# Optimization experiments

Hardware: AMD Instinct MI355X
Metric: run time of the kernel (lower is better)

## Reference

```python
import jax, jax.numpy as jnp
import numpy as np

B, IN_C, H, W = 32, 256, 32, 32
C_OUT, NUM_MODES, NEG_MODES, EMB = 256, 1, 3, 512
SIGMA, BETA, NEG_SCOPE, EPS = 0.5, 0.3, 2.0, 1e-12


def _l2norm(v, axis):
    return v / jnp.maximum(jnp.linalg.norm(v, axis=axis, keepdims=True), EPS)


def setup_inputs() -> dict:
    key = jax.random.key(0)
    ks = jax.random.split(key, 6)
    x = jax.random.normal(ks[0], (B, IN_C, H, W), jnp.float32)
    W_emb = jax.random.normal(ks[1], (EMB, IN_C), jnp.float32) * 0.02  # 1x1 conv kernel
    # rep_fc / neg_rep_fc: nn.Linear(1, C*modes*E), normal_init std=0.01
    rep_w = jax.random.normal(ks[2], (C_OUT * NUM_MODES * EMB, 1), jnp.float32) * 0.01
    rep_b = jax.random.normal(ks[3], (C_OUT * NUM_MODES * EMB,), jnp.float32) * 0.01
    neg_rep_w = jax.random.normal(ks[4], (C_OUT * NEG_MODES * EMB, 1), jnp.float32) * 0.01
    neg_rep_b = jax.random.normal(ks[5], (C_OUT * NEG_MODES * EMB,), jnp.float32) * 0.01
    return {"x": x, "W_emb": W_emb, "rep_w": rep_w, "rep_b": rep_b,
            "neg_rep_w": neg_rep_w, "neg_rep_b": neg_rep_b}


def reference(x, W_emb, rep_w, rep_b, neg_rep_w, neg_rep_b):
    # emb_module: 1x1 conv, then L2-normalize over channel dim (dim=1)
    emb = jnp.einsum('bchw,ec->behw', x, W_emb)
    emb = _l2norm(emb, axis=1)                                    # [B,E,H,W], unit-norm over E
    # training branch: reps = normalize(rep_fc(1.0)) = normalize(w*1 + b)
    reps = _l2norm((rep_w[:, 0] + rep_b).reshape(C_OUT, NUM_MODES, EMB), axis=2)
    reps_neg = _l2norm((neg_rep_w[:, 0] + neg_rep_b).reshape(C_OUT, NEG_MODES, EMB), axis=2)

    def dist(r):
        # ||e - r||^2 = ||e||^2 + ||r||^2 - 2 e.r = 2 - 2 e.r (both unit-norm)
        dot = jnp.einsum('behw,cme->bcmhw', emb, r)               # [B,C,M,H,W]
        return jnp.sqrt(jnp.maximum(2.0 - 2.0 * dot, 0.0))

    distances = dist(reps)                                        # [B,C,1,H,W]
    distances_neg = dist(reps_neg)                                # [B,C,3,H,W]
    inv2s2 = 1.0 / (2.0 * SIGMA ** 2)

    probs_neg = jnp.exp(-distances_neg ** 2 * inv2s2)
    cls_score_neg = probs_neg.max(axis=2)                         # [B,C,H,W]
    probs_ori = jnp.exp(-distances ** 2 * inv2s2).max(axis=2)     # [B,C,H,W]

    neg_min = distances_neg.min(axis=2, keepdims=True)            # [B,C,1,H,W]
    probs = jnp.exp(-(distances + BETA * jax.nn.relu(NEG_SCOPE - neg_min)) ** 2 * inv2s2)
    # cls_norm=True branch
    probs_sumj = probs.sum(axis=2)                                # [B,C,H,W]
    cls_score = probs_sumj / probs_sumj.sum(axis=1, keepdims=True)
    return (cls_score, cls_score_neg, distances, distances_neg, probs_ori)
```

## Files before the change

### kernel.cpp

```cpp
#include <hip/hip_runtime.h>
#include <stdint.h>

using s16x8 = __attribute__((ext_vector_type(8))) short;
using f32x4 = __attribute__((ext_vector_type(4))) float;

#define HW 1024
#define INC 256
#define EMB 512
#define NPX 32768

#define OFF_CS 0
#define OFF_CN 8388608
#define OFF_D  16777216
#define OFF_DN 25165824
#define OFF_PO 50331648

__device__ __forceinline__ uint32_t f2bf(float f) {
  uint32_t u = __float_as_uint(f);
  return (u + 0x7FFFu + ((u >> 16) & 1u)) >> 16;
}
__device__ __forceinline__ int lswz(int row, int byte) {
  return byte ^ (((row >> 2) & 7) << 4);
}

__global__ __launch_bounds__(64) void k_prep(
    const float* __restrict__ rep_w, const float* __restrict__ rep_b,
    const float* __restrict__ neg_w, const float* __restrict__ neg_b,
    uint16_t* __restrict__ R) {
  int rb = blockIdx.x, lane = threadIdx.x;
  int c = rb >> 2, md = rb & 3;
  const float* w  = (md == 0) ? rep_w : neg_w;
  const float* bb = (md == 0) ? rep_b : neg_b;
  int base = (md == 0) ? c * EMB : (c * 3 + md - 1) * EMB;
  float v[8]; float ss = 0.f;
#pragma unroll
  for (int j = 0; j < 8; ++j) {
    float t = w[base + lane * 8 + j] + bb[base + lane * 8 + j];
    v[j] = t; ss += t * t;
  }
#pragma unroll
  for (int o = 1; o < 64; o <<= 1) ss += __shfl_xor(ss, o, 64);
  float inv = 1.f / fmaxf(sqrtf(ss), 1e-12f);
  uint16_t* dst = R + rb * EMB + lane * 8;
#pragma unroll
  for (int j = 0; j < 8; ++j) dst[j] = (uint16_t)f2bf(v[j] * inv);
}

__global__ __launch_bounds__(256) void k_gemm1(
    const float* __restrict__ x, const float* __restrict__ wemb,
    uint16_t* __restrict__ emb, float* __restrict__ nparts) {
  int bid = blockIdx.x;
  int w = (bid & 7) * 128 + (bid >> 3);
  int e_tile = w & 3, px_tile = w >> 2;
  int e0 = e_tile * 128, px0 = px_tile * 128;
  int bimg = px0 >> 10, hw0 = px0 & 1023;
  int tid = threadIdx.x, lane = tid & 63, wid = tid >> 6;
  int wm = wid >> 1, wn = wid & 1, lr = lane & 15, lk = lane >> 4;
  __shared__ __align__(16) char smA[16384];
  __shared__ __align__(16) char smB[16384];
  f32x4 acc[4][4] = {};
  const float4* x4 = (const float4*)x;
  const float4* w4 = (const float4*)wemb;
  for (int kt = 0; kt < INC; kt += 64) {
    if (kt) __syncthreads();
#pragma unroll
    for (int i = 0; i < 4; ++i) {
      int p = tid + i * 256;
      int c2 = p >> 5, px4 = p & 31;
      int gi = ((bimg * INC + kt + c2 * 2) * HW + hw0) >> 2;
      float4 fa = x4[gi + px4];
      float4 fb = x4[gi + 256 + px4];
      float fa_[4] = {fa.x, fa.y, fa.z, fa.w};
      float fb_[4] = {fb.x, fb.y, fb.z, fb.w};
#pragma unroll
      for (int j = 0; j < 4; ++j) {
        int px = px4 * 4 + j;
        uint32_t val = f2bf(fa_[j]) | (f2bf(fb_[j]) << 16);
        *(uint32_t*)(smA + px * 128 + lswz(px, c2 * 4)) = val;
      }
    }
#pragma unroll
    for (int i = 0; i < 8; ++i) {
      int q = tid + i * 256;
      int er = q >> 4, c4 = q & 15;
      float4 f = w4[(((e0 + er) * INC + kt) >> 2) + c4];
      uint2 val;
      val.x = f2bf(f.x) | (f2bf(f.y) << 16);
      val.y = f2bf(f.z) | (f2bf(f.w) << 16);
      *(uint2*)(smB + er * 128 + lswz(er, c4 * 8)) = val;
    }
    __syncthreads();
#pragma unroll
    for (int kk = 0; kk < 64; kk += 32) {
      s16x8 a[4], b[4];
#pragma unroll
      for (int mi = 0; mi < 4; ++mi) {
        int row = wm * 64 + mi * 16 + lr;
        a[mi] = *(const s16x8*)(smA + row * 128 + lswz(row, (kk + lk * 8) * 2));
      }
#pragma unroll
      for (int ni = 0; ni < 4; ++ni) {
        int row = wn * 64 + ni * 16 + lr;
        b[ni] = *(const s16x8*)(smB + row * 128 + lswz(row, (kk + lk * 8) * 2));
      }
#pragma unroll
      for (int mi = 0; mi < 4; ++mi)
#pragma unroll
        for (int ni = 0; ni < 4; ++ni)
          acc[mi][ni] = __builtin_amdgcn_mfma_f32_16x16x32_bf16(a[mi], b[ni], acc[mi][ni], 0, 0, 0);
    }
  }
#pragma unroll
  for (int mi = 0; mi < 4; ++mi) {
#pragma unroll
    for (int r = 0; r < 4; ++r) {
      int pxg = px0 + wm * 64 + mi * 16 + lk * 4 + r;
      float ss = 0.f;
#pragma unroll
      for (int ni = 0; ni < 4; ++ni) {
        float v = acc[mi][ni][r];
        ss += v * v;
        uint32_t bf = f2bf(v);
        uint32_t other = (uint32_t)__shfl_xor((int)bf, 1, 64);
        if (!(lane & 1)) {
          int e = e0 + wn * 64 + ni * 16 + lr;
          *(uint32_t*)(emb + pxg * EMB + e) = bf | (other << 16);
        }
      }
      ss += __shfl_xor(ss, 1, 64);
      ss += __shfl_xor(ss, 2, 64);
      ss += __shfl_xor(ss, 4, 64);
      ss += __shfl_xor(ss, 8, 64);
      if (lr == 0) nparts[(e_tile * 2 + wn) * NPX + pxg] = ss;
    }
  }
}

__global__ __launch_bounds__(256) void k_gemm2(
    const uint16_t* __restrict__ Rm, const uint16_t* __restrict__ emb,
    const float* __restrict__ nparts, float* __restrict__ out,
    float* __restrict__ psum_part) {
  int bid = blockIdx.x;
  int w = (bid & 7) * 256 + (bid >> 3);
  int px_tile = w >> 3, rep_tile = w & 7;
  int px0 = px_tile * 128, r0 = rep_tile * 128;
  int bimg = px0 >> 10;
  int tid = threadIdx.x, lane = tid & 63, wid = tid >> 6;
  int wm = wid >> 1, wn = wid & 1, lr = lane & 15, lk = lane >> 4;
  __shared__ __align__(16) char ep_s[4 * 1184];
  f32x4 acc[4][4] = {};
  const char* Ab = (const char*)Rm  + (r0  + wm * 64 + lr) * 1024 + lk * 16;
  const char* Bb = (const char*)emb + (px0 + wn * 64 + lr) * 1024 + lk * 16;
#pragma unroll
  for (int ks = 0; ks < 16; ++ks) {
    s16x8 a[4], b[4];
#pragma unroll
    for (int mi = 0; mi < 4; ++mi)
      a[mi] = *(const s16x8*)(Ab + mi * 16384 + ks * 64);
#pragma unroll
    for (int ni = 0; ni < 4; ++ni)
      b[ni] = *(const s16x8*)(Bb + ni * 16384 + ks * 64);
#pragma unroll
    for (int mi = 0; mi < 4; ++mi)
#pragma unroll
      for (int ni = 0; ni < 4; ++ni)
        acc[mi][ni] = __builtin_amdgcn_mfma_f32_16x16x32_bf16(a[mi], b[ni], acc[mi][ni], 0, 0, 0);
  }
  char* ep = ep_s + wid * 1184;
  int hwbase = (px0 & 1023) + wn * 64;
  int obase = (bimg * 256) * HW + hwbase;
  float invn[4], psacc[4];
#pragma unroll
  for (int ni = 0; ni < 4; ++ni) {
    int px = px0 + wn * 64 + ni * 16 + lr;
    float s = 0.f;
#pragma unroll
    for (int t = 0; t < 8; ++t) s += nparts[t * NPX + px];
    invn[ni] = rsqrtf(fmaxf(s, 1e-24f));
    psacc[ni] = 0.f;
  }
#pragma unroll
  for (int mi = 0; mi < 4; ++mi) {
    int clsl = wm * 16 + mi * 4 + lk;
    int cls = (r0 >> 2) + clsl;
    float pl[7][4];
#pragma unroll
    for (int ni = 0; ni < 4; ++ni) {
      float in = invn[ni];
      float d0 = acc[mi][ni][0] * in;
      float d1 = acc[mi][ni][1] * in;
      float d2 = acc[mi][ni][2] * in;
      float d3 = acc[mi][ni][3] * in;
      float q0 = fmaxf(2.f - 2.f * d0, 0.f);
      float q1 = fmaxf(2.f - 2.f * d1, 0.f);
      float q2 = fmaxf(2.f - 2.f * d2, 0.f);
      float q3 = fmaxf(2.f - 2.f * d3, 0.f);
      float dist0 = sqrtf(q0);
      float qmin = fminf(q1, fminf(q2, q3));
      float negmin = sqrtf(qmin);
      float pen = 0.3f * fmaxf(2.f - negmin, 0.f);
      float tt = dist0 + pen;
      float probs = __expf(-2.f * tt * tt);
      pl[0][ni] = probs;
      pl[1][ni] = __expf(-2.f * qmin);
      pl[2][ni] = dist0;
      pl[3][ni] = sqrtf(q1);
      pl[4][ni] = sqrtf(q2);
      pl[5][ni] = sqrtf(q3);
      pl[6][ni] = __expf(-2.f * q0);
      psacc[ni] += probs;
    }
    int bc = obase + cls * HW;
    int bn = OFF_DN + (bimg * 768 + cls * 3) * HW + hwbase;
    int pbase[7] = { OFF_CS + bc, OFF_CN + bc, OFF_D + bc,
                     bn, bn + HW, bn + 2 * HW, OFF_PO + bc };
#pragma unroll
    for (int p = 0; p < 7; ++p) {
#pragma unroll
      for (int ni = 0; ni < 4; ++ni)
        *(float*)(ep + lk * 288 + (ni * 16 + lr) * 4) = pl[p][ni];
      float4 v = *(const float4*)(ep + lk * 288 + lr * 16);
      *(float4*)(&out[pbase[p] + 4 * lr]) = v;
    }
  }
#pragma unroll
  for (int ni = 0; ni < 4; ++ni) {
    float s = psacc[ni];
    s += __shfl_xor(s, 16, 64);
    s += __shfl_xor(s, 32, 64);
    if (lk == 0)
      psum_part[(rep_tile * 2 + wm) * NPX + px0 + wn * 64 + ni * 16 + lr] = s;
  }
}

__global__ __launch_bounds__(256) void k_psum(const float* __restrict__ psum_part,
                                              float* __restrict__ inv_ps) {
  int px = blockIdx.x * 256 + threadIdx.x;
  float s = 0.f;
#pragma unroll
  for (int t = 0; t < 16; ++t) s += psum_part[t * NPX + px];
  inv_ps[px] = 1.f / s;
}

__global__ __launch_bounds__(256) void k_norm(float* __restrict__ out,
                                              const float* __restrict__ inv_ps) {
  int idx4 = blockIdx.x * 256 + threadIdx.x;
  int base = idx4 << 2;
  int b = base >> 18, hw = base & 1023;
  float4 p = *(const float4*)&inv_ps[(b << 10) | hw];
  float4* o4 = (float4*)out;
  float4 v = o4[idx4];
  v.x *= p.x; v.y *= p.y; v.z *= p.z; v.w *= p.w;
  o4[idx4] = v;
}

extern "C" void kernel_launch(void* const* d_in, const int* in_sizes, int n_in,
                              void* d_out, int out_size, void* d_ws, size_t ws_size,
                              hipStream_t stream) {
  (void)in_sizes; (void)n_in; (void)out_size; (void)ws_size;
  const float* x     = (const float*)d_in[0];
  const float* wemb  = (const float*)d_in[1];
  const float* rep_w = (const float*)d_in[2];
  const float* rep_b = (const float*)d_in[3];
  const float* neg_w = (const float*)d_in[4];
  const float* neg_b = (const float*)d_in[5];
  float* out = (float*)d_out;
  char* ws = (char*)d_ws;
  uint16_t* R         = (uint16_t*)ws;
  float*    nparts    = (float*)(ws + (1 << 20));
  float*    psum_part = (float*)(ws + (2 << 20));
  float*    inv_ps    = (float*)(ws + (4 << 20));
  uint16_t* emb       = (uint16_t*)(ws + (5 << 20));
  hipLaunchKernelGGL(k_prep,  dim3(1024), dim3(64),  0, stream,
                     rep_w, rep_b, neg_w, neg_b, R);
  hipLaunchKernelGGL(k_gemm1, dim3(1024), dim3(256), 0, stream, x, wemb, emb, nparts);
  hipLaunchKernelGGL(k_gemm2, dim3(2048), dim3(256), 0, stream, R, emb, nparts, out, psum_part);
  hipLaunchKernelGGL(k_psum,  dim3(128),  dim3(256), 0, stream, psum_part, inv_ps);
  hipLaunchKernelGGL(k_norm,  dim3(8192), dim3(256), 0, stream, out, inv_ps);
}
```

Measured before the change: 446.6 us.

## Fuse embedding GEMM, distance GEMM and partial-sum into one kernel with LDS-resident embeddings

Result: faster. 389.9 us (-12.7%).

```diff
diff --git a/kernel.cpp b/kernel.cpp
--- a/kernel.cpp
+++ b/kernel.cpp
@@ -7,7 +7,6 @@
 #define HW 1024
 #define INC 256
 #define EMB 512
-#define NPX 32768
 
 #define OFF_CS 0
 #define OFF_CN 8388608
@@ -46,28 +45,39 @@
   for (int j = 0; j < 8; ++j) dst[j] = (uint16_t)f2bf(v[j] * inv);
 }
 
-__global__ __launch_bounds__(256) void k_gemm1(
+__global__ __launch_bounds__(512, 2) void k_fused(
     const float* __restrict__ x, const float* __restrict__ wemb,
-    uint16_t* __restrict__ emb, float* __restrict__ nparts) {
-  int bid = blockIdx.x;
-  int w = (bid & 7) * 128 + (bid >> 3);
-  int e_tile = w & 3, px_tile = w >> 2;
-  int e0 = e_tile * 128, px0 = px_tile * 128;
-  int bimg = px0 >> 10, hw0 = px0 & 1023;
+    const uint16_t* __restrict__ Rm, float* __restrict__ out,
+    float* __restrict__ inv_ps) {
+  __shared__ __align__(16) char L[155648];
+  char* embS = L;
+  char* smA  = L + 73728;
+  char* smB  = L + 90112;
+  char* Rbuf = L + 131072;
+  float* nrm = (float*)(L + 147456);
+  float* psl = (float*)(L + 131072);
+
+  int bx = blockIdx.x;
+  int px0 = bx * 128, bimg = bx >> 3, hw0 = px0 & 1023;
   int tid = threadIdx.x, lane = tid & 63, wid = tid >> 6;
-  int wm = wid >> 1, wn = wid & 1, lr = lane & 15, lk = lane >> 4;
-  __shared__ __align__(16) char smA[16384];
-  __shared__ __align__(16) char smB[16384];
-  f32x4 acc[4][4] = {};
+  int lr = lane & 15, lk = lane >> 4;
+
+  int rrow = tid >> 2, rsl = tid & 3;
+  const char* Rb = (const char*)Rm;
+  uint4 rs0 = *(const uint4*)(Rb + rrow * 1024 + rsl * 16);
+  uint4 rs1 = *(const uint4*)(Rb + rrow * 1024 + rsl * 16 + 64);
+
+  int wm1 = wid >> 2, wn1 = wid & 3;
+  f32x4 acc1[4][8] = {};
   const float4* x4 = (const float4*)x;
   const float4* w4 = (const float4*)wemb;
-  for (int kt = 0; kt < INC; kt += 64) {
-    if (kt) __syncthreads();
-#pragma unroll
-    for (int i = 0; i < 4; ++i) {
-      int p = tid + i * 256;
+  for (int ck = 0; ck < INC; ck += 64) {
+    if (ck) __syncthreads();
+#pragma unroll
+    for (int i = 0; i < 2; ++i) {
+      int p = tid + i * 512;
       int c2 = p >> 5, px4 = p & 31;
-      int gi = ((bimg * INC + kt + c2 * 2) * HW + hw0) >> 2;
+      int gi = ((bimg * INC + ck + c2 * 2) * HW + hw0) >> 2;
       float4 fa = x4[gi + px4];
       float4 fb = x4[gi + 256 + px4];
       float fa_[4] = {fa.x, fa.y, fa.z, fa.w};
@@ -80,10 +90,10 @@
       }
     }
 #pragma unroll
-    for (int i = 0; i < 8; ++i) {
-      int q = tid + i * 256;
+    for (int i = 0; i < 16; ++i) {
+      int q = tid + i * 512;
       int er = q >> 4, c4 = q & 15;
-      float4 f = w4[(((e0 + er) * INC + kt) >> 2) + c4];
+      float4 f = w4[er * 64 + (ck >> 2) + c4];
       uint2 val;
       val.x = f2bf(f.x) | (f2bf(f.y) << 16);
       val.y = f2bf(f.z) | (f2bf(f.w) << 16);
@@ -92,154 +102,144 @@
     __syncthreads();
 #pragma unroll
     for (int kk = 0; kk < 64; kk += 32) {
-      s16x8 a[4], b[4];
+      s16x8 a[4], b[8];
 #pragma unroll
       for (int mi = 0; mi < 4; ++mi) {
-        int row = wm * 64 + mi * 16 + lr;
+        int row = wm1 * 64 + mi * 16 + lr;
         a[mi] = *(const s16x8*)(smA + row * 128 + lswz(row, (kk + lk * 8) * 2));
       }
 #pragma unroll
-      for (int ni = 0; ni < 4; ++ni) {
-        int row = wn * 64 + ni * 16 + lr;
+      for (int ni = 0; ni < 8; ++ni) {
+        int row = wn1 * 128 + ni * 16 + lr;
         b[ni] = *(const s16x8*)(smB + row * 128 + lswz(row, (kk + lk * 8) * 2));
       }
 #pragma unroll
       for (int mi = 0; mi < 4; ++mi)
 #pragma unroll
-        for (int ni = 0; ni < 4; ++ni)
-          acc[mi][ni] = __builtin_amdgcn_mfma_f32_16x16x32_bf16(a[mi], b[ni], acc[mi][ni], 0, 0, 0);
-    }
-  }
+        for (int ni = 0; ni < 8; ++ni)
+          acc1[mi][ni] = __builtin_amdgcn_mfma_f32_16x16x32_bf16(a[mi], b[ni], acc1[mi][ni], 0, 0, 0);
+    }
+  }
+  __syncthreads();
 #pragma unroll
   for (int mi = 0; mi < 4; ++mi) {
 #pragma unroll
     for (int r = 0; r < 4; ++r) {
-      int pxg = px0 + wm * 64 + mi * 16 + lk * 4 + r;
+      int px = wm1 * 64 + mi * 16 + lk * 4 + r;
       float ss = 0.f;
 #pragma unroll
-      for (int ni = 0; ni < 4; ++ni) {
-        float v = acc[mi][ni][r];
+      for (int ni = 0; ni < 8; ++ni) {
+        float v = acc1[mi][ni][r];
         ss += v * v;
         uint32_t bf = f2bf(v);
         uint32_t other = (uint32_t)__shfl_xor((int)bf, 1, 64);
         if (!(lane & 1)) {
-          int e = e0 + wn * 64 + ni * 16 + lr;
-          *(uint32_t*)(emb + pxg * EMB + e) = bf | (other << 16);
+          int ebyte = wn1 * 256 + ni * 32 + lr * 2;
+          *(uint32_t*)(embS + px * 1024 + (ebyte ^ ((px & 7) << 4))) = bf | (other << 16);
         }
       }
       ss += __shfl_xor(ss, 1, 64);
       ss += __shfl_xor(ss, 2, 64);
       ss += __shfl_xor(ss, 4, 64);
       ss += __shfl_xor(ss, 8, 64);
-      if (lr == 0) nparts[(e_tile * 2 + wn) * NPX + pxg] = ss;
-    }
-  }
-}
-
-__global__ __launch_bounds__(256) void k_gemm2(
-    const uint16_t* __restrict__ Rm, const uint16_t* __restrict__ emb,
-    const float* __restrict__ nparts, float* __restrict__ out,
-    float* __restrict__ psum_part) {
-  int bid = blockIdx.x;
-  int w = (bid & 7) * 256 + (bid >> 3);
-  int px_tile = w >> 3, rep_tile = w & 7;
-  int px0 = px_tile * 128, r0 = rep_tile * 128;
-  int bimg = px0 >> 10;
-  int tid = threadIdx.x, lane = tid & 63, wid = tid >> 6;
-  int wm = wid >> 1, wn = wid & 1, lr = lane & 15, lk = lane >> 4;
-  __shared__ __align__(16) char ep_s[4 * 1184];
-  f32x4 acc[4][4] = {};
-  const char* Ab = (const char*)Rm  + (r0  + wm * 64 + lr) * 1024 + lk * 16;
-  const char* Bb = (const char*)emb + (px0 + wn * 64 + lr) * 1024 + lk * 16;
-#pragma unroll
-  for (int ks = 0; ks < 16; ++ks) {
-    s16x8 a[4], b[4];
-#pragma unroll
-    for (int mi = 0; mi < 4; ++mi)
-      a[mi] = *(const s16x8*)(Ab + mi * 16384 + ks * 64);
-#pragma unroll
-    for (int ni = 0; ni < 4; ++ni)
-      b[ni] = *(const s16x8*)(Bb + ni * 16384 + ks * 64);
-#pragma unroll
-    for (int mi = 0; mi < 4; ++mi)
-#pragma unroll
-      for (int ni = 0; ni < 4; ++ni)
-        acc[mi][ni] = __builtin_amdgcn_mfma_f32_16x16x32_bf16(a[mi], b[ni], acc[mi][ni], 0, 0, 0);
-  }
-  char* ep = ep_s + wid * 1184;
-  int hwbase = (px0 & 1023) + wn * 64;
-  int obase = (bimg * 256) * HW + hwbase;
-  float invn[4], psacc[4];
-#pragma unroll
-  for (int ni = 0; ni < 4; ++ni) {
-    int px = px0 + wn * 64 + ni * 16 + lr;
-    float s = 0.f;
-#pragma unroll
-    for (int t = 0; t < 8; ++t) s += nparts[t * NPX + px];
-    invn[ni] = rsqrtf(fmaxf(s, 1e-24f));
-    psacc[ni] = 0.f;
-  }
-#pragma unroll
-  for (int mi = 0; mi < 4; ++mi) {
-    int clsl = wm * 16 + mi * 4 + lk;
-    int cls = (r0 >> 2) + clsl;
-    float pl[7][4];
-#pragma unroll
-    for (int ni = 0; ni < 4; ++ni) {
-      float in = invn[ni];
-      float d0 = acc[mi][ni][0] * in;
-      float d1 = acc[mi][ni][1] * in;
-      float d2 = acc[mi][ni][2] * in;
-      float d3 = acc[mi][ni][3] * in;
-      float q0 = fmaxf(2.f - 2.f * d0, 0.f);
-      float q1 = fmaxf(2.f - 2.f * d1, 0.f);
-      float q2 = fmaxf(2.f - 2.f * d2, 0.f);
-      float q3 = fmaxf(2.f - 2.f * d3, 0.f);
-      float dist0 = sqrtf(q0);
-      float qmin = fminf(q1, fminf(q2, q3));
-      float negmin = sqrtf(qmin);
-      float pen = 0.3f * fmaxf(2.f - negmin, 0.f);
-      float tt = dist0 + pen;
-      float probs = __expf(-2.f * tt * tt);
-      pl[0][ni] = probs;
-      pl[1][ni] = __expf(-2.f * qmin);
-      pl[2][ni] = dist0;
-      pl[3][ni] = sqrtf(q1);
-      pl[4][ni] = sqrtf(q2);
-      pl[5][ni] = sqrtf(q3);
-      pl[6][ni] = __expf(-2.f * q0);
-      psacc[ni] += probs;
-    }
-    int bc = obase + cls * HW;
-    int bn = OFF_DN + (bimg * 768 + cls * 3) * HW + hwbase;
-    int pbase[7] = { OFF_CS + bc, OFF_CN + bc, OFF_D + bc,
-                     bn, bn + HW, bn + 2 * HW, OFF_PO + bc };
-#pragma unroll
-    for (int p = 0; p < 7; ++p) {
-#pragma unroll
-      for (int ni = 0; ni < 4; ++ni)
-        *(float*)(ep + lk * 288 + (ni * 16 + lr) * 4) = pl[p][ni];
-      float4 v = *(const float4*)(ep + lk * 288 + lr * 16);
-      *(float4*)(&out[pbase[p] + 4 * lr]) = v;
-    }
-  }
-#pragma unroll
-  for (int ni = 0; ni < 4; ++ni) {
-    float s = psacc[ni];
-    s += __shfl_xor(s, 16, 64);
-    s += __shfl_xor(s, 32, 64);
-    if (lk == 0)
-      psum_part[(rep_tile * 2 + wm) * NPX + px0 + wn * 64 + ni * 16 + lr] = s;
-  }
-}
-
-__global__ __launch_bounds__(256) void k_psum(const float* __restrict__ psum_part,
-                                              float* __restrict__ inv_ps) {
-  int px = blockIdx.x * 256 + threadIdx.x;
-  float s = 0.f;
-#pragma unroll
-  for (int t = 0; t < 16; ++t) s += psum_part[t * NPX + px];
-  inv_ps[px] = 1.f / s;
+      if (lr == 0) nrm[wn1 * 128 + px] = ss;
+    }
+  }
+  __syncthreads();
+
+  int wm2 = wid >> 2, wn2 = wid & 3;
+  float invn2[2];
+#pragma unroll
+  for (int bi = 0; bi < 2; ++bi) {
+    int px = wn2 * 32 + bi * 16 + lr;
+    float s = nrm[px] + nrm[128 + px] + nrm[256 + px] + nrm[384 + px];
+    invn2[bi] = rsqrtf(fmaxf(s, 1e-24f));
+  }
+  f32x4 acc2[4][2] = {};
+  float ps0 = 0.f, ps1 = 0.f;
+  int hwb = hw0 + wn2 * 32;
+  for (int c = 0; c < 64; ++c) {
+    __syncthreads();
+    int wb = rrow * 128, wsz = (rrow & 7) << 4;
+    *(uint4*)(Rbuf + wb + ((rsl * 16) ^ wsz)) = rs0;
+    *(uint4*)(Rbuf + wb + ((rsl * 16 + 64) ^ wsz)) = rs1;
+    __syncthreads();
+    if (c < 63) {
+      int cn = c + 1;
+      const char* src = Rb + ((cn >> 3) * 128 + rrow) * 1024 + (cn & 7) * 128 + rsl * 16;
+      rs0 = *(const uint4*)(src);
+      rs1 = *(const uint4*)(src + 64);
+    }
+    int kt = c & 7;
+#pragma unroll
+    for (int ks = 0; ks < 2; ++ks) {
+      s16x8 a[4], b[2];
+#pragma unroll
+      for (int ai = 0; ai < 4; ++ai) {
+        int row = wm2 * 64 + ai * 16 + lr;
+        a[ai] = *(const s16x8*)(Rbuf + row * 128 + ((ks * 64 + lk * 16) ^ ((row & 7) << 4)));
+      }
+#pragma unroll
+      for (int bi = 0; bi < 2; ++bi) {
+        int px = wn2 * 32 + bi * 16 + lr;
+        b[bi] = *(const s16x8*)(embS + px * 1024 + ((kt * 128 + ks * 64 + lk * 16) ^ ((px & 7) << 4)));
+      }
+#pragma unroll
+      for (int ai = 0; ai < 4; ++ai)
+#pragma unroll
+        for (int bi = 0; bi < 2; ++bi)
+          acc2[ai][bi] = __builtin_amdgcn_mfma_f32_16x16x32_bf16(a[ai], b[bi], acc2[ai][bi], 0, 0, 0);
+    }
+    if (kt == 7) {
+      int rc = c >> 3;
+#pragma unroll
+      for (int ai = 0; ai < 4; ++ai) {
+        int cls = rc * 32 + wm2 * 16 + ai * 4 + lk;
+        int bc = ((bimg << 8) + cls) << 10;
+        int bn = OFF_DN + ((bimg * 768 + cls * 3) << 10);
+#pragma unroll
+        for (int bi = 0; bi < 2; ++bi) {
+          float in = invn2[bi];
+          int hw = hwb + bi * 16 + lr;
+          float d0 = acc2[ai][bi][0] * in;
+          float d1 = acc2[ai][bi][1] * in;
+          float d2 = acc2[ai][bi][2] * in;
+          float d3 = acc2[ai][bi][3] * in;
+          float q0 = fmaxf(2.f - 2.f * d0, 0.f);
+          float q1 = fmaxf(2.f - 2.f * d1, 0.f);
+          float q2 = fmaxf(2.f - 2.f * d2, 0.f);
+          float q3 = fmaxf(2.f - 2.f * d3, 0.f);
+          float dist0 = sqrtf(q0);
+          float qmin = fminf(q1, fminf(q2, q3));
+          float negmin = sqrtf(qmin);
+          float pen = 0.3f * fmaxf(2.f - negmin, 0.f);
+          float tt = dist0 + pen;
+          float probs = __expf(-2.f * tt * tt);
+          out[OFF_CS + bc + hw] = probs;
+          out[OFF_CN + bc + hw] = __expf(-2.f * qmin);
+          out[OFF_D  + bc + hw] = dist0;
+          out[OFF_PO + bc + hw] = __expf(-2.f * q0);
+          out[bn + hw]        = sqrtf(q1);
+          out[bn + 1024 + hw] = sqrtf(q2);
+          out[bn + 2048 + hw] = sqrtf(q3);
+          if (bi == 0) ps0 += probs; else ps1 += probs;
+          acc2[ai][bi] = (f32x4){0.f, 0.f, 0.f, 0.f};
+        }
+      }
+    }
+  }
+  ps0 += __shfl_xor(ps0, 16, 64); ps0 += __shfl_xor(ps0, 32, 64);
+  ps1 += __shfl_xor(ps1, 16, 64); ps1 += __shfl_xor(ps1, 32, 64);
+  __syncthreads();
+  if (lk == 0) {
+    psl[wm2 * 128 + wn2 * 32 + lr] = ps0;
+    psl[wm2 * 128 + wn2 * 32 + 16 + lr] = ps1;
+  }
+  __syncthreads();
+  if (tid < 128) {
+    float s = psl[tid] + psl[128 + tid];
+    inv_ps[px0 + tid] = 1.f / s;
+  }
 }
 
 __global__ __launch_bounds__(256) void k_norm(float* __restrict__ out,
@@ -266,15 +266,10 @@
   const float* neg_b = (const float*)d_in[5];
   float* out = (float*)d_out;
   char* ws = (char*)d_ws;
-  uint16_t* R         = (uint16_t*)ws;
-  float*    nparts    = (float*)(ws + (1 << 20));
-  float*    psum_part = (float*)(ws + (2 << 20));
-  float*    inv_ps    = (float*)(ws + (4 << 20));
-  uint16_t* emb       = (uint16_t*)(ws + (5 << 20));
+  uint16_t* R      = (uint16_t*)ws;
+  float*    inv_ps = (float*)(ws + (1 << 20));
   hipLaunchKernelGGL(k_prep,  dim3(1024), dim3(64),  0, stream,
                      rep_w, rep_b, neg_w, neg_b, R);
-  hipLaunchKernelGGL(k_gemm1, dim3(1024), dim3(256), 0, stream, x, wemb, emb, nparts);
-  hipLaunchKernelGGL(k_gemm2, dim3(2048), dim3(256), 0, stream, R, emb, nparts, out, psum_part);
-  hipLaunchKernelGGL(k_psum,  dim3(128),  dim3(256), 0, stream, psum_part, inv_ps);
+  hipLaunchKernelGGL(k_fused, dim3(256),  dim3(512), 0, stream, x, wemb, R, out, inv_ps);
   hipLaunchKernelGGL(k_norm,  dim3(8192), dim3(256), 0, stream, out, inv_ps);
 }
```
